# Optimization experiments

Measured on AMD Instinct MI355X. Metric: run time of the kernel, lower is better.

The kernel has to match this reference:

```python
import jax, jax.numpy as jnp
import numpy as np

N_NODES = 50000
N_EDGES = 800000
NODE_DIM = 128
EDGE_DIM = 128
HIDDEN = 128
GATE_DIM = 2


def _mlp(x, w1, b1, w2, b2):
    # Linear -> ReLU -> Linear (assumed 2-layer MLP(in, out, hidden))
    return jax.nn.relu(x @ w1.T + b1) @ w2.T + b2


def _init_linear(key, out_d, in_d, scale=0.02):
    return (jax.random.normal(key, (out_d, in_d), dtype=jnp.float32) * scale)


def setup_inputs() -> dict:
    key = jax.random.key(0)
    ks = jax.random.split(key, 32)
    inp = {}
    inp["h_node"] = jax.random.normal(ks[0], (N_NODES, NODE_DIM), dtype=jnp.float32)
    inp["h_edge"] = jax.random.normal(ks[1], (N_EDGES, EDGE_DIM), dtype=jnp.float32)
    inp["edge_index"] = jax.random.randint(ks[2], (2, N_EDGES), 0, N_NODES, dtype=jnp.int64)
    inp["relative_vec"] = jax.random.normal(ks[3], (N_EDGES, 3), dtype=jnp.float32)
    inp["distance"] = jax.random.uniform(ks[4], (N_EDGES,), dtype=jnp.float32)
    inp["node_extra"] = jax.random.normal(ks[5], (N_NODES, GATE_DIM), dtype=jnp.float32)
    # left_lin_edge: MLP(node_dim, node_dim, hidden)
    inp["left_w1"] = _init_linear(ks[6], HIDDEN, NODE_DIM)
    inp["left_b1"] = jnp.zeros((HIDDEN,), jnp.float32)
    inp["left_w2"] = _init_linear(ks[7], NODE_DIM, HIDDEN)
    inp["left_b2"] = jnp.zeros((NODE_DIM,), jnp.float32)
    # right_lin_edge: MLP(node_dim, node_dim, hidden)
    inp["right_w1"] = _init_linear(ks[8], HIDDEN, NODE_DIM)
    inp["right_b1"] = jnp.zeros((HIDDEN,), jnp.float32)
    inp["right_w2"] = _init_linear(ks[9], NODE_DIM, HIDDEN)
    inp["right_b2"] = jnp.zeros((NODE_DIM,), jnp.float32)
    # BondFFN(edge_dim, node_dim*2, inter_dim=node_dim, gate_dim, out_dim=1)
    inp["bond_lin_w"] = _init_linear(ks[10], NODE_DIM, EDGE_DIM)           # bond_linear (no bias)
    inp["nodeb_lin_w"] = _init_linear(ks[11], NODE_DIM, 2 * NODE_DIM)      # node_linear (no bias)
    inp["inter_w1"] = _init_linear(ks[12], NODE_DIM, NODE_DIM)             # inter MLP(node_dim,1,node_dim)
    inp["inter_b1"] = jnp.zeros((NODE_DIM,), jnp.float32)
    inp["inter_w2"] = _init_linear(ks[13], 1, NODE_DIM)
    inp["inter_b2"] = jnp.zeros((1,), jnp.float32)
    gate_in = EDGE_DIM + 2 * NODE_DIM + GATE_DIM                            # 386
    inp["gate_w1"] = _init_linear(ks[14], 32, gate_in)                     # gate MLP(gate_in,1,32)
    inp["gate_b1"] = jnp.zeros((32,), jnp.float32)
    inp["gate_w2"] = _init_linear(ks[15], 1, 32)
    inp["gate_b2"] = jnp.zeros((1,), jnp.float32)
    # pos_scale_net: MLP(node_dim+1+2, 1, hidden) -> sigmoid
    inp["scale_w1"] = _init_linear(ks[16], HIDDEN, NODE_DIM + 1 + GATE_DIM)
    inp["scale_b1"] = jnp.zeros((HIDDEN,), jnp.float32)
    inp["scale_w2"] = _init_linear(ks[17], 1, HIDDEN)
    inp["scale_b2"] = jnp.zeros((1,), jnp.float32)
    return inp


def reference(h_node, h_edge, edge_index, relative_vec, distance, node_extra,
              left_w1, left_b1, left_w2, left_b2,
              right_w1, right_b1, right_w2, right_b2,
              bond_lin_w, nodeb_lin_w,
              inter_w1, inter_b1, inter_w2, inter_b2,
              gate_w1, gate_b1, gate_w2, gate_b2,
              scale_w1, scale_b1, scale_w2, scale_b2):
    el, er = edge_index[0], edge_index[1]
    # gather + per-edge node MLPs
    left_feat = _mlp(h_node[el], left_w1, left_b1, left_w2, left_b2)    # [E, node_dim]
    right_feat = _mlp(h_node[er], right_w1, right_b1, right_w2, right_b2)
    both_extra = node_extra[el]                                         # [E, gate_dim]
    node_cat = jnp.concatenate([left_feat, right_feat], axis=-1)        # [E, 2*node_dim]
    # BondFFN
    inter_feat = h_edge @ bond_lin_w.T + node_cat @ nodeb_lin_w.T       # [E, node_dim]
    inter_feat = _mlp(inter_feat, inter_w1, inter_b1, inter_w2, inter_b2)  # [E, 1]
    gate = _mlp(jnp.concatenate([h_edge, node_cat, both_extra], axis=-1),
                gate_w1, gate_b1, gate_w2, gate_b2)                     # [E, 1]
    weight_edge = inter_feat * jax.nn.sigmoid(gate)                     # [E, 1]
    d = distance[:, None]
    force_edge = weight_edge * relative_vec / (d + 1e-6) / (d + 5.0) * 5  # [E, 3]
    # scatter_sum over left node index
    delta_pos = jax.ops.segment_sum(force_edge, el, num_segments=h_node.shape[0])  # [N, 3]
    nrm = jnp.linalg.norm(delta_pos, axis=-1, keepdims=True)
    scale = jax.nn.sigmoid(_mlp(jnp.concatenate([h_node, node_extra, nrm], axis=-1),
                                scale_w1, scale_b1, scale_w2, scale_b2))  # [N, 1]
    return delta_pos * scale
```

## Files before the change

### kernel.cpp

```cpp
#include <hip/hip_runtime.h>
#include <math.h>

#define N_NODES 50000
#define N_EDGES 800000

using bf16x8 = __attribute__((ext_vector_type(8))) short;
using f32x4  = __attribute__((ext_vector_type(4))) float;
typedef unsigned short u16;
typedef unsigned int   u32;

__device__ __forceinline__ u16 f2bf(float f) {
    union { float f; u32 u; } v; v.f = f;
    u32 u = v.u + 0x7fffu + ((v.u >> 16) & 1u);
    return (u16)(u >> 16);
}
__device__ __forceinline__ float bf2f(u32 h) {
    union { u32 u; float f; } v; v.u = h << 16;
    return v.f;
}

#define SA_LD 136
#define SW_LD 40

template<bool RELU>
__global__ __launch_bounds__(256, 4)
void mfma_gemm(const u16* __restrict__ A, int lda,
               const u16* __restrict__ W, int ldw,
               const float* __restrict__ bias,
               u16* __restrict__ C, int ldc,
               int M, int N, int K)
{
    __shared__ u16 sA[64 * SW_LD];
    __shared__ u16 sW[64 * SW_LD];
    const int tid = threadIdx.x;
    const int w = tid >> 6, lane = tid & 63, lx = lane & 15, quad = lane >> 4;
    const int m0 = blockIdx.x * 64, n0 = blockIdx.y * 64;

    f32x4 acc[4];
#pragma unroll
    for (int nt = 0; nt < 4; ++nt) {
        float b = bias ? bias[n0 + nt * 16 + lx] : 0.f;
        f32x4 t; t[0] = b; t[1] = b; t[2] = b; t[3] = b; acc[nt] = t;
    }

    const int sr = tid >> 2;
    const int sseg = (tid & 3) * 8;
    const int ksteps = K >> 5;
    for (int ks = 0; ks < ksteps; ++ks) {
        const int k0 = ks * 32;
        __syncthreads();
        int am = m0 + sr; if (am >= M) am = M - 1;
        uint4 va = *(const uint4*)&A[(size_t)am * lda + k0 + sseg];
        *(uint4*)&sA[sr * SW_LD + sseg] = va;
        uint4 vw = *(const uint4*)&W[(size_t)(n0 + sr) * ldw + k0 + sseg];
        *(uint4*)&sW[sr * SW_LD + sseg] = vw;
        __syncthreads();
        bf16x8 af = *(const bf16x8*)&sA[(w * 16 + lx) * SW_LD + quad * 8];
#pragma unroll
        for (int nt = 0; nt < 4; ++nt) {
            bf16x8 bf = *(const bf16x8*)&sW[(nt * 16 + lx) * SW_LD + quad * 8];
            acc[nt] = __builtin_amdgcn_mfma_f32_16x16x32_bf16(af, bf, acc[nt], 0, 0, 0);
        }
    }
#pragma unroll
    for (int r = 0; r < 4; ++r) {
        int m = m0 + w * 16 + quad * 4 + r;
        if (m >= M) continue;
#pragma unroll
        for (int nt = 0; nt < 4; ++nt) {
            float v = acc[nt][r];
            if (RELU) v = fmaxf(v, 0.f);
            C[(size_t)m * ldc + n0 + nt * 16 + lx] = f2bf(v);
        }
    }
}

__global__ void conv_hnode(const float* __restrict__ src, u16* __restrict__ dst)
{
    int idx = blockIdx.x * 256 + threadIdx.x;
    if (idx >= N_NODES * 32) return;
    float4 v = ((const float4*)src)[idx];
    uint2 o;
    o.x = (u32)f2bf(v.x) | ((u32)f2bf(v.y) << 16);
    o.y = (u32)f2bf(v.z) | ((u32)f2bf(v.w) << 16);
    *(uint2*)&dst[(size_t)idx * 4] = o;
}

__global__ void prep_small(const float* lw1, const float* rw1,
                           const float* lb1, const float* rb1,
                           const float* bond_w, const float* iw1, const float* gw1,
                           const float* sw1,
                           u16* W1cat, float* b1cat, u16* bond_bf, u16* iw1_bf,
                           u16* gate_bf, u16* sw1c)
{
    int idx = blockIdx.x * 256 + threadIdx.x;
    if (idx < 32768) {
        int i = idx >> 7, k = idx & 127;
        float v = (i < 128) ? lw1[i * 128 + k] : rw1[(i - 128) * 128 + k];
        W1cat[idx] = f2bf(v);
    } else if (idx < 33024) {
        int i = idx - 32768;
        b1cat[i] = (i < 128) ? lb1[i] : rb1[i - 128];
    } else if (idx < 49408) {
        int t = idx - 33024;
        bond_bf[t] = f2bf(bond_w[t]);
    } else if (idx < 65792) {
        int t = idx - 49408;
        iw1_bf[t] = f2bf(iw1[t]);
    } else if (idx < 69888) {
        int t = idx - 65792;
        int g = t >> 7, k = t & 127;
        gate_bf[t] = f2bf(gw1[(size_t)g * 386 + k]);
    } else if (idx < 90368) {
        int t = idx - 69888;
        int o = t / 160, k = t % 160;
        sw1c[t] = (k < 131) ? f2bf(sw1[(size_t)o * 131 + k]) : (u16)0;
    }
}

__global__ void compose_wp(const float* __restrict__ nodeb_w, const float* __restrict__ gw1,
                           const float* __restrict__ lw2, const float* __restrict__ rw2,
                           const float* __restrict__ lb2, const float* __restrict__ rb2,
                           const float* __restrict__ gb1,
                           u16* __restrict__ WP, float* __restrict__ bP)
{
    int idx = blockIdx.x * 256 + threadIdx.x;
    if (idx >= 320 * 256) return;
    int i = idx >> 8;
    int j = idx & 255;
    bool leftRow = (i < 160);
    bool leftK = (j < 128);
    if (leftRow != leftK) { WP[idx] = 0; return; }

    const float* src;
    const float* w2 = leftRow ? lw2 : rw2;
    const float* b2 = leftRow ? lb2 : rb2;
    float biasExtra = 0.f;
    if (i < 128) {
        int c = ((i & 7) << 4) + (i >> 3);
        src = nodeb_w + (size_t)c * 256;
    } else if (i < 160) {
        int r = i - 128, g = ((r & 1) << 4) + (r >> 1);
        src = gw1 + (size_t)g * 386 + 128;
        biasExtra = gb1[g];
    } else if (i < 288) {
        int r = i - 160, c = ((r & 7) << 4) + (r >> 3);
        src = nodeb_w + (size_t)c * 256 + 128;
    } else {
        int r = i - 288, g = ((r & 1) << 4) + (r >> 1);
        src = gw1 + (size_t)g * 386 + 256;
    }
    int jj = j & 127;
    float s = 0.f;
#pragma unroll 4
    for (int k = 0; k < 128; ++k)
        s += src[k] * w2[(size_t)k * 128 + jj];
    WP[idx] = f2bf(s);
    if (jj == 0) {
        float b = biasExtra;
        for (int k = 0; k < 128; ++k) b += src[k] * b2[k];
        bP[i] = b;
    }
}

__global__ void fix_glx(u16* __restrict__ P, const float* __restrict__ ne,
                        const float* __restrict__ gw1)
{
    int idx = blockIdx.x * 256 + threadIdx.x;
    if (idx >= N_NODES * 32) return;
    int n = idx >> 5, g = idx & 31;
    int pos = ((g & 15) << 1) + (g >> 4);
    u16* p = &P[(size_t)n * 320 + 128 + pos];
    float v = bf2f(*p) + ne[n * 2] * gw1[(size_t)g * 386 + 384]
                       + ne[n * 2 + 1] * gw1[(size_t)g * 386 + 385];
    *p = f2bf(v);
}

__global__ __launch_bounds__(256, 4)
void edge_kernel(const float* __restrict__ he,
                 const int*   __restrict__ eidx,
                 const float* __restrict__ rel_vec,
                 const float* __restrict__ dist,
                 const u16*   __restrict__ P,
                 const u16*   __restrict__ bondw,
                 const u16*   __restrict__ iw1w,
                 const u16*   __restrict__ gatew,
                 const float* __restrict__ ib1,
                 const float* __restrict__ iw2,
                 const float* __restrict__ ib2,
                 const float* __restrict__ gw2,
                 const float* __restrict__ gb2,
                 float* __restrict__ dp)
{
    __shared__ u16 sA[64 * SA_LD];
    __shared__ u16 sW[128 * SW_LD];
    __shared__ u16 sWg[32 * SW_LD];
    __shared__ int sEL[64], sER[64];
    __shared__ float sG[64], sIS[64];

    const int tid = threadIdx.x;
    const int w = tid >> 6, lane = tid & 63, lx = lane & 15, quad = lane >> 4;
    const int eb = blockIdx.x * 64;

    if (tid < 64) { sEL[tid] = eidx[eb + tid]; sER[tid] = eidx[N_EDGES + eb + tid]; }

#pragma unroll
    for (int j = 0; j < 8; ++j) {
        int fid = j * 256 + tid;
        int e = fid >> 5, kq = (fid & 31) << 2;
        float4 v = *(const float4*)&he[(size_t)(eb + e) * 128 + kq];
        uint2 o;
        o.x = (u32)f2bf(v.x) | ((u32)f2bf(v.y) << 16);
        o.y = (u32)f2bf(v.z) | ((u32)f2bf(v.w) << 16);
        *(uint2*)&sA[e * SA_LD + kq] = o;
    }

    f32x4 acc[8], accg[2];
#pragma unroll
    for (int i = 0; i < 8; ++i) { f32x4 z; z[0]=0;z[1]=0;z[2]=0;z[3]=0; acc[i] = z; }
    { f32x4 z; z[0]=0;z[1]=0;z[2]=0;z[3]=0; accg[0] = z; accg[1] = z; }

    const int wrow = tid >> 1;
    const int wseg = (tid & 1) * 16;

    for (int ks = 0; ks < 4; ++ks) {
        const int k0 = ks * 32;
        __syncthreads();
        {
            uint4 v0 = *(const uint4*)&bondw[wrow * 128 + k0 + wseg];
            uint4 v1 = *(const uint4*)&bondw[wrow * 128 + k0 + wseg + 8];
            *(uint4*)&sW[wrow * SW_LD + wseg] = v0;
            *(uint4*)&sW[wrow * SW_LD + wseg + 8] = v1;
            if (tid < 64) {
                uint4 g0 = *(const uint4*)&gatew[wrow * 128 + k0 + wseg];
                uint4 g1 = *(const uint4*)&gatew[wrow * 128 + k0 + wseg + 8];
                *(uint4*)&sWg[wrow * SW_LD + wseg] = g0;
                *(uint4*)&sWg[wrow * SW_LD + wseg + 8] = g1;
            }
        }
        __syncthreads();
        bf16x8 af = *(const bf16x8*)&sA[(w * 16 + lx) * SA_LD + k0 + quad * 8];
#pragma unroll
        for (int nt = 0; nt < 8; ++nt) {
            bf16x8 bf = *(const bf16x8*)&sW[(nt * 16 + lx) * SW_LD + quad * 8];
            acc[nt] = __builtin_amdgcn_mfma_f32_16x16x32_bf16(af, bf, acc[nt], 0, 0, 0);
        }
#pragma unroll
        for (int nt = 0; nt < 2; ++nt) {
            bf16x8 bf = *(const bf16x8*)&sWg[(nt * 16 + lx) * SW_LD + quad * 8];
            accg[nt] = __builtin_amdgcn_mfma_f32_16x16x32_bf16(af, bf, accg[nt], 0, 0, 0);
        }
    }

    {
        float gw2a = gw2[lx], gw2b = gw2[16 + lx];
        float gb2v = gb2[0];
#pragma unroll
        for (int r = 0; r < 4; ++r) {
            int erow = w * 16 + quad * 4 + r;
            size_t lbase = (size_t)sEL[erow] * 320;
            size_t rbase = (size_t)sER[erow] * 320 + 160;
            u32 gl = *(const u32*)&P[lbase + 128 + lx * 2];
            u32 gr = *(const u32*)&P[rbase + 128 + lx * 2];
            float g0 = bf2f(gl & 0xffff) + bf2f(gr & 0xffff);
            float g1 = bf2f(gl >> 16) + bf2f(gr >> 16);
            float v = fmaxf(accg[0][r] + g0, 0.f) * gw2a
                    + fmaxf(accg[1][r] + g1, 0.f) * gw2b;
            v += __shfl_xor(v, 1); v += __shfl_xor(v, 2);
            v += __shfl_xor(v, 4); v += __shfl_xor(v, 8);
            if (lx == 0) sG[erow] = 1.f / (1.f + __expf(-(v + gb2v)));
        }
    }

    __syncthreads();

#pragma unroll
    for (int r = 0; r < 4; ++r) {
        int erow = w * 16 + quad * 4 + r;
        size_t lbase = (size_t)sEL[erow] * 320;
        size_t rbase = (size_t)sER[erow] * 320 + 160;
        uint4 lv = *(const uint4*)&P[lbase + lx * 8];
        uint4 rv = *(const uint4*)&P[rbase + lx * 8];
        const u32* lw_ = (const u32*)&lv;
        const u32* rw_ = (const u32*)&rv;
#pragma unroll
        for (int nt = 0; nt < 8; ++nt) {
            u32 lh = (nt & 1) ? (lw_[nt >> 1] >> 16) : (lw_[nt >> 1] & 0xffff);
            u32 rh = (nt & 1) ? (rw_[nt >> 1] >> 16) : (rw_[nt >> 1] & 0xffff);
            float tv = acc[nt][r] + bf2f(lh) + bf2f(rh);
            sA[erow * SA_LD + nt * 16 + lx] = f2bf(tv);
        }
    }
#pragma unroll
    for (int nt = 0; nt < 8; ++nt) {
        float b = ib1[nt * 16 + lx];
        f32x4 t; t[0] = b; t[1] = b; t[2] = b; t[3] = b; acc[nt] = t;
    }
    __syncthreads();

    for (int ks = 0; ks < 4; ++ks) {
        const int k0 = ks * 32;
        __syncthreads();
        {
            uint4 v0 = *(const uint4*)&iw1w[wrow * 128 + k0 + wseg];
            uint4 v1 = *(const uint4*)&iw1w[wrow * 128 + k0 + wseg + 8];
            *(uint4*)&sW[wrow * SW_LD + wseg] = v0;
            *(uint4*)&sW[wrow * SW_LD + wseg + 8] = v1;
        }
        __syncthreads();
        bf16x8 af = *(const bf16x8*)&sA[(w * 16 + lx) * SA_LD + k0 + quad * 8];
#pragma unroll
        for (int nt = 0; nt < 8; ++nt) {
            bf16x8 bf = *(const bf16x8*)&sW[(nt * 16 + lx) * SW_LD + quad * 8];
            acc[nt] = __builtin_amdgcn_mfma_f32_16x16x32_bf16(af, bf, acc[nt], 0, 0, 0);
        }
    }

    {
        float ib2v = ib2[0];
        float iw2v[8];
#pragma unroll
        for (int nt = 0; nt < 8; ++nt) iw2v[nt] = iw2[nt * 16 + lx];
#pragma unroll
        for (int r = 0; r < 4; ++r) {
            float v = 0.f;
#pragma unroll
            for (int nt = 0; nt < 8; ++nt)
                v += fmaxf(acc[nt][r], 0.f) * iw2v[nt];
            v += __shfl_xor(v, 1); v += __shfl_xor(v, 2);
            v += __shfl_xor(v, 4); v += __shfl_xor(v, 8);
            if (lx == 0) sIS[w * 16 + quad * 4 + r] = v + ib2v;
        }
    }
    __syncthreads();

    if (tid < 64) {
        float wgt = sIS[tid] * sG[tid];
        float d = dist[eb + tid];
        float coef = 5.f * wgt / ((d + 1e-6f) * (d + 5.f));
        const float* rv = &rel_vec[(size_t)(eb + tid) * 3];
        int n = sEL[tid];
        atomicAdd(&dp[n * 3 + 0], coef * rv[0]);
        atomicAdd(&dp[n * 3 + 1], coef * rv[1]);
        atomicAdd(&dp[n * 3 + 2], coef * rv[2]);
    }
}

__global__ void build_xc(u16* __restrict__ Xc, const float* __restrict__ h_node,
                         const float* __restrict__ ne, const float* __restrict__ dp)
{
    int idx = blockIdx.x * 256 + threadIdx.x;
    if (idx >= N_NODES * 160) return;
    int n = idx / 160, c = idx % 160;
    float v;
    if (c < 128) v = h_node[(size_t)n * 128 + c];
    else if (c == 128) v = ne[n * 2];
    else if (c == 129) v = ne[n * 2 + 1];
    else if (c == 130) {
        float x = dp[n * 3], y = dp[n * 3 + 1], z = dp[n * 3 + 2];
        v = sqrtf(x * x + y * y + z * z);
    } else v = 0.f;
    Xc[idx] = f2bf(v);
}

__global__ __launch_bounds__(256)
void finalize(const u16* __restrict__ U, const float* __restrict__ sw2,
              const float* __restrict__ sb2, const float* __restrict__ dp,
              float* __restrict__ out)
{
    int node = blockIdx.x * 4 + (threadIdx.x >> 6);
    int lane = threadIdx.x & 63;
    const u16* u = &U[(size_t)node * 128];
    float p = bf2f(u[lane]) * sw2[lane] + bf2f(u[lane + 64]) * sw2[lane + 64];
    p += __shfl_xor(p, 1);  p += __shfl_xor(p, 2);
    p += __shfl_xor(p, 4);  p += __shfl_xor(p, 8);
    p += __shfl_xor(p, 16); p += __shfl_xor(p, 32);
    if (lane == 0) {
        float s = 1.f / (1.f + __expf(-(p + sb2[0])));
        out[node * 3 + 0] = dp[node * 3 + 0] * s;
        out[node * 3 + 1] = dp[node * 3 + 1] * s;
        out[node * 3 + 2] = dp[node * 3 + 2] * s;
    }
}

extern "C" void kernel_launch(void* const* d_in, const int* in_sizes, int n_in,
                              void* d_out, int out_size, void* d_ws, size_t ws_size,
                              hipStream_t stream)
{
    const float* h_node  = (const float*)d_in[0];
    const float* h_edge  = (const float*)d_in[1];
    const int*   eidx    = (const int*)  d_in[2];
    const float* rel_vec = (const float*)d_in[3];
    const float* dist    = (const float*)d_in[4];
    const float* ne      = (const float*)d_in[5];
    const float* lw1 = (const float*)d_in[6];  const float* lb1 = (const float*)d_in[7];
    const float* lw2 = (const float*)d_in[8];  const float* lb2 = (const float*)d_in[9];
    const float* rw1 = (const float*)d_in[10]; const float* rb1 = (const float*)d_in[11];
    const float* rw2 = (const float*)d_in[12]; const float* rb2 = (const float*)d_in[13];
    const float* bond_w  = (const float*)d_in[14];
    const float* nodeb_w = (const float*)d_in[15];
    const float* iw1 = (const float*)d_in[16]; const float* ib1 = (const float*)d_in[17];
    const float* iw2 = (const float*)d_in[18]; const float* ib2 = (const float*)d_in[19];
    const float* gw1 = (const float*)d_in[20]; const float* gb1 = (const float*)d_in[21];
    const float* gw2 = (const float*)d_in[22]; const float* gb2 = (const float*)d_in[23];
    const float* sw1 = (const float*)d_in[24]; const float* sb1 = (const float*)d_in[25];
    const float* sw2 = (const float*)d_in[26]; const float* sb2 = (const float*)d_in[27];
    float* out = (float*)d_out;

    char* base = (char*)d_ws;
    auto carve = [&](size_t bytes) { char* p = base; base += (bytes + 255) & ~(size_t)255; return p; };
    u16*  hnode_bf = (u16*) carve((size_t)N_NODES * 128 * 2);
    u16*  H1       = (u16*) carve((size_t)N_NODES * 256 * 2);
    u16*  P        = (u16*) carve((size_t)N_NODES * 320 * 2);
    u16*  Xc       = (u16*) carve((size_t)N_NODES * 160 * 2);
    u16*  U        = (u16*) carve((size_t)N_NODES * 128 * 2);
    u16*  W1cat    = (u16*) carve(256 * 128 * 2);
    u16*  WP       = (u16*) carve(320 * 256 * 2);
    u16*  bond_bf  = (u16*) carve(128 * 128 * 2);
    u16*  iw1_bf   = (u16*) carve(128 * 128 * 2);
    u16*  gate_bf  = (u16*) carve(32 * 128 * 2);
    u16*  sw1c     = (u16*) carve(128 * 160 * 2);
    float* b1cat   = (float*)carve(256 * 4);
    float* bP      = (float*)carve(320 * 4);
    float* dp      = (float*)carve((size_t)N_NODES * 3 * 4);

    hipMemsetAsync(dp, 0, (size_t)N_NODES * 3 * 4, stream);

    dim3 blk(256);
    conv_hnode<<<(N_NODES * 32 + 255) / 256, blk, 0, stream>>>(h_node, hnode_bf);
    prep_small<<<(90368 + 255) / 256, blk, 0, stream>>>(lw1, rw1, lb1, rb1, bond_w, iw1, gw1, sw1,
                                                        W1cat, b1cat, bond_bf, iw1_bf, gate_bf, sw1c);
    compose_wp<<<320, blk, 0, stream>>>(nodeb_w, gw1, lw2, rw2, lb2, rb2, gb1, WP, bP);

    const int MB = (N_NODES + 63) / 64;
    mfma_gemm<true ><<<dim3(MB, 4), blk, 0, stream>>>(hnode_bf, 128, W1cat, 128, b1cat, H1, 256, N_NODES, 256, 128);
    mfma_gemm<false><<<dim3(MB, 5), blk, 0, stream>>>(H1, 256, WP, 256, bP, P, 320, N_NODES, 320, 256);
    fix_glx<<<(N_NODES * 32 + 255) / 256, blk, 0, stream>>>(P, ne, gw1);

    edge_kernel<<<N_EDGES / 64, blk, 0, stream>>>(h_edge, eidx, rel_vec, dist, P,
                                                  bond_bf, iw1_bf, gate_bf,
                                                  ib1, iw2, ib2, gw2, gb2, dp);

    build_xc<<<(N_NODES * 160 + 255) / 256, blk, 0, stream>>>(Xc, h_node, ne, dp);
    mfma_gemm<true ><<<dim3(MB, 2), blk, 0, stream>>>(Xc, 160, sw1c, 160, sb1, U, 128, N_NODES, 128, 160);
    finalize<<<N_NODES / 4, blk, 0, stream>>>(U, sw2, sb2, dp, out);
}
```

Measured before the change: 839.5 us.

## Pre-swizzle edge weights to MFMA fragment layout and load whole matrices once

The bond, inter and gate weight matrices are stored in a fragment-ordered layout so each lane reads contiguous 16-byte chunks. Each matrix is loaded into shared memory once per block, which removes the per-k-step syncs and reloads. The edge block grows to 128 edges with 512 threads, and the gathers of node features from P are issued early so they overlap the first GEMM. The scatter is split across three threads per edge, one per coordinate. This raises LDS usage per block and register pressure, which may lower occupancy.

```diff
diff --git a/kernel.cpp b/kernel.cpp
--- a/kernel.cpp
+++ b/kernel.cpp
@@ -103,14 +103,22 @@
         b1cat[i] = (i < 128) ? lb1[i] : rb1[i - 128];
     } else if (idx < 49408) {
         int t = idx - 33024;
-        bond_bf[t] = f2bf(bond_w[t]);
+        int e = t & 7, lx = (t >> 3) & 15, quad = (t >> 7) & 3;
+        int ks = (t >> 9) & 3, g = t >> 11;
+        int n = g * 16 + lx, k = ks * 32 + quad * 8 + e;
+        bond_bf[t] = f2bf(bond_w[n * 128 + k]);
     } else if (idx < 65792) {
         int t = idx - 49408;
-        iw1_bf[t] = f2bf(iw1[t]);
+        int e = t & 7, lx = (t >> 3) & 15, quad = (t >> 7) & 3;
+        int ks = (t >> 9) & 3, g = t >> 11;
+        int n = g * 16 + lx, k = ks * 32 + quad * 8 + e;
+        iw1_bf[t] = f2bf(iw1[n * 128 + k]);
     } else if (idx < 69888) {
         int t = idx - 65792;
-        int g = t >> 7, k = t & 127;
-        gate_bf[t] = f2bf(gw1[(size_t)g * 386 + k]);
+        int e = t & 7, lx = (t >> 3) & 15, quad = (t >> 7) & 3;
+        int ks = (t >> 9) & 3, g = t >> 11;
+        int n = g * 16 + lx, k = ks * 32 + quad * 8 + e;
+        gate_bf[t] = f2bf(gw1[(size_t)n * 386 + k]);
     } else if (idx < 90368) {
         int t = idx - 69888;
         int o = t / 160, k = t % 160;
@@ -176,7 +184,7 @@
     *p = f2bf(v);
 }
 
-__global__ __launch_bounds__(256, 4)
+__global__ __launch_bounds__(512, 4)
 void edge_kernel(const float* __restrict__ he,
                  const int*   __restrict__ eidx,
                  const float* __restrict__ rel_vec,
@@ -192,21 +200,27 @@
                  const float* __restrict__ gb2,
                  float* __restrict__ dp)
 {
-    __shared__ u16 sA[64 * SA_LD];
-    __shared__ u16 sW[128 * SW_LD];
-    __shared__ u16 sWg[32 * SW_LD];
-    __shared__ int sEL[64], sER[64];
-    __shared__ float sG[64], sIS[64];
+    __shared__ u16 sA[128 * SA_LD];
+    __shared__ u16 sW[16384 + 4096];
+    __shared__ int sEL[128], sER[128];
+    __shared__ float sG[128], sIS[128];
 
     const int tid = threadIdx.x;
     const int w = tid >> 6, lane = tid & 63, lx = lane & 15, quad = lane >> 4;
-    const int eb = blockIdx.x * 64;
-
-    if (tid < 64) { sEL[tid] = eidx[eb + tid]; sER[tid] = eidx[N_EDGES + eb + tid]; }
+    const int eb = blockIdx.x * 128;
+
+    if (tid < 128) { sEL[tid] = eidx[eb + tid]; sER[tid] = eidx[N_EDGES + eb + tid]; }
+
+#pragma unroll
+    for (int j = 0; j < 4; ++j) {
+        int t = j * 512 + tid;
+        *(uint4*)&sW[t * 8] = *(const uint4*)&bondw[t * 8];
+    }
+    *(uint4*)&sW[16384 + tid * 8] = *(const uint4*)&gatew[tid * 8];
 
 #pragma unroll
     for (int j = 0; j < 8; ++j) {
-        int fid = j * 256 + tid;
+        int fid = j * 512 + tid;
         int e = fid >> 5, kq = (fid & 31) << 2;
         float4 v = *(const float4*)&he[(size_t)(eb + e) * 128 + kq];
         uint2 o;
@@ -214,40 +228,36 @@
         o.y = (u32)f2bf(v.z) | ((u32)f2bf(v.w) << 16);
         *(uint2*)&sA[e * SA_LD + kq] = o;
     }
+    __syncthreads();
+
+    uint4 lv[4], rv[4]; u32 gl[4], gr[4];
+#pragma unroll
+    for (int r = 0; r < 4; ++r) {
+        int erow = w * 16 + quad * 4 + r;
+        size_t lbase = (size_t)sEL[erow] * 320;
+        size_t rbase = (size_t)sER[erow] * 320 + 160;
+        lv[r] = *(const uint4*)&P[lbase + lx * 8];
+        rv[r] = *(const uint4*)&P[rbase + lx * 8];
+        gl[r] = *(const u32*)&P[lbase + 128 + lx * 2];
+        gr[r] = *(const u32*)&P[rbase + 128 + lx * 2];
+    }
 
     f32x4 acc[8], accg[2];
 #pragma unroll
     for (int i = 0; i < 8; ++i) { f32x4 z; z[0]=0;z[1]=0;z[2]=0;z[3]=0; acc[i] = z; }
     { f32x4 z; z[0]=0;z[1]=0;z[2]=0;z[3]=0; accg[0] = z; accg[1] = z; }
 
-    const int wrow = tid >> 1;
-    const int wseg = (tid & 1) * 16;
-
+#pragma unroll
     for (int ks = 0; ks < 4; ++ks) {
-        const int k0 = ks * 32;
-        __syncthreads();
-        {
-            uint4 v0 = *(const uint4*)&bondw[wrow * 128 + k0 + wseg];
-            uint4 v1 = *(const uint4*)&bondw[wrow * 128 + k0 + wseg + 8];
-            *(uint4*)&sW[wrow * SW_LD + wseg] = v0;
-            *(uint4*)&sW[wrow * SW_LD + wseg + 8] = v1;
-            if (tid < 64) {
-                uint4 g0 = *(const uint4*)&gatew[wrow * 128 + k0 + wseg];
-                uint4 g1 = *(const uint4*)&gatew[wrow * 128 + k0 + wseg + 8];
-                *(uint4*)&sWg[wrow * SW_LD + wseg] = g0;
-                *(uint4*)&sWg[wrow * SW_LD + wseg + 8] = g1;
-            }
-        }
-        __syncthreads();
-        bf16x8 af = *(const bf16x8*)&sA[(w * 16 + lx) * SA_LD + k0 + quad * 8];
+        bf16x8 af = *(const bf16x8*)&sA[(w * 16 + lx) * SA_LD + ks * 32 + quad * 8];
 #pragma unroll
         for (int nt = 0; nt < 8; ++nt) {
-            bf16x8 bf = *(const bf16x8*)&sW[(nt * 16 + lx) * SW_LD + quad * 8];
+            bf16x8 bf = *(const bf16x8*)&sW[((nt * 4 + ks) << 9) + lane * 8];
             acc[nt] = __builtin_amdgcn_mfma_f32_16x16x32_bf16(af, bf, acc[nt], 0, 0, 0);
         }
 #pragma unroll
         for (int nt = 0; nt < 2; ++nt) {
-            bf16x8 bf = *(const bf16x8*)&sWg[(nt * 16 + lx) * SW_LD + quad * 8];
+            bf16x8 bf = *(const bf16x8*)&sW[16384 + ((nt * 4 + ks) << 9) + lane * 8];
             accg[nt] = __builtin_amdgcn_mfma_f32_16x16x32_bf16(af, bf, accg[nt], 0, 0, 0);
         }
     }
@@ -257,32 +267,21 @@
         float gb2v = gb2[0];
 #pragma unroll
         for (int r = 0; r < 4; ++r) {
-            int erow = w * 16 + quad * 4 + r;
-            size_t lbase = (size_t)sEL[erow] * 320;
-            size_t rbase = (size_t)sER[erow] * 320 + 160;
-            u32 gl = *(const u32*)&P[lbase + 128 + lx * 2];
-            u32 gr = *(const u32*)&P[rbase + 128 + lx * 2];
-            float g0 = bf2f(gl & 0xffff) + bf2f(gr & 0xffff);
-            float g1 = bf2f(gl >> 16) + bf2f(gr >> 16);
+            float g0 = bf2f(gl[r] & 0xffff) + bf2f(gr[r] & 0xffff);
+            float g1 = bf2f(gl[r] >> 16) + bf2f(gr[r] >> 16);
             float v = fmaxf(accg[0][r] + g0, 0.f) * gw2a
                     + fmaxf(accg[1][r] + g1, 0.f) * gw2b;
             v += __shfl_xor(v, 1); v += __shfl_xor(v, 2);
             v += __shfl_xor(v, 4); v += __shfl_xor(v, 8);
-            if (lx == 0) sG[erow] = 1.f / (1.f + __expf(-(v + gb2v)));
-        }
-    }
-
-    __syncthreads();
+            if (lx == 0) sG[w * 16 + quad * 4 + r] = 1.f / (1.f + __expf(-(v + gb2v)));
+        }
+    }
 
 #pragma unroll
     for (int r = 0; r < 4; ++r) {
         int erow = w * 16 + quad * 4 + r;
-        size_t lbase = (size_t)sEL[erow] * 320;
-        size_t rbase = (size_t)sER[erow] * 320 + 160;
-        uint4 lv = *(const uint4*)&P[lbase + lx * 8];
-        uint4 rv = *(const uint4*)&P[rbase + lx * 8];
-        const u32* lw_ = (const u32*)&lv;
-        const u32* rw_ = (const u32*)&rv;
+        const u32* lw_ = (const u32*)&lv[r];
+        const u32* rw_ = (const u32*)&rv[r];
 #pragma unroll
         for (int nt = 0; nt < 8; ++nt) {
             u32 lh = (nt & 1) ? (lw_[nt >> 1] >> 16) : (lw_[nt >> 1] & 0xffff);
@@ -296,22 +295,21 @@
         float b = ib1[nt * 16 + lx];
         f32x4 t; t[0] = b; t[1] = b; t[2] = b; t[3] = b; acc[nt] = t;
     }
+
     __syncthreads();
-
+#pragma unroll
+    for (int j = 0; j < 4; ++j) {
+        int t = j * 512 + tid;
+        *(uint4*)&sW[t * 8] = *(const uint4*)&iw1w[t * 8];
+    }
+    __syncthreads();
+
+#pragma unroll
     for (int ks = 0; ks < 4; ++ks) {
-        const int k0 = ks * 32;
-        __syncthreads();
-        {
-            uint4 v0 = *(const uint4*)&iw1w[wrow * 128 + k0 + wseg];
-            uint4 v1 = *(const uint4*)&iw1w[wrow * 128 + k0 + wseg + 8];
-            *(uint4*)&sW[wrow * SW_LD + wseg] = v0;
-            *(uint4*)&sW[wrow * SW_LD + wseg + 8] = v1;
-        }
-        __syncthreads();
-        bf16x8 af = *(const bf16x8*)&sA[(w * 16 + lx) * SA_LD + k0 + quad * 8];
+        bf16x8 af = *(const bf16x8*)&sA[(w * 16 + lx) * SA_LD + ks * 32 + quad * 8];
 #pragma unroll
         for (int nt = 0; nt < 8; ++nt) {
-            bf16x8 bf = *(const bf16x8*)&sW[(nt * 16 + lx) * SW_LD + quad * 8];
+            bf16x8 bf = *(const bf16x8*)&sW[((nt * 4 + ks) << 9) + lane * 8];
             acc[nt] = __builtin_amdgcn_mfma_f32_16x16x32_bf16(af, bf, acc[nt], 0, 0, 0);
         }
     }
@@ -334,15 +332,14 @@
     }
     __syncthreads();
 
-    if (tid < 64) {
-        float wgt = sIS[tid] * sG[tid];
-        float d = dist[eb + tid];
-        float coef = 5.f * wgt / ((d + 1e-6f) * (d + 5.f));
-        const float* rv = &rel_vec[(size_t)(eb + tid) * 3];
-        int n = sEL[tid];
-        atomicAdd(&dp[n * 3 + 0], coef * rv[0]);
-        atomicAdd(&dp[n * 3 + 1], coef * rv[1]);
-        atomicAdd(&dp[n * 3 + 2], coef * rv[2]);
+    {
+        int e = tid >> 2, c = tid & 3;
+        if (c < 3) {
+            float wgt = sIS[e] * sG[e];
+            float d = dist[eb + e];
+            float coef = 5.f * wgt / ((d + 1e-6f) * (d + 5.f));
+            atomicAdd(&dp[sEL[e] * 3 + c], coef * rel_vec[(size_t)(eb + e) * 3 + c]);
+        }
     }
 }
 
@@ -437,9 +434,9 @@
     mfma_gemm<false><<<dim3(MB, 5), blk, 0, stream>>>(H1, 256, WP, 256, bP, P, 320, N_NODES, 320, 256);
     fix_glx<<<(N_NODES * 32 + 255) / 256, blk, 0, stream>>>(P, ne, gw1);
 
-    edge_kernel<<<N_EDGES / 64, blk, 0, stream>>>(h_edge, eidx, rel_vec, dist, P,
-                                                  bond_bf, iw1_bf, gate_bf,
-                                                  ib1, iw2, ib2, gw2, gb2, dp);
+    edge_kernel<<<N_EDGES / 128, dim3(512), 0, stream>>>(h_edge, eidx, rel_vec, dist, P,
+                                                         bond_bf, iw1_bf, gate_bf,
+                                                         ib1, iw2, ib2, gw2, gb2, dp);
 
     build_xc<<<(N_NODES * 160 + 255) / 256, blk, 0, stream>>>(Xc, h_node, ne, dp);
     mfma_gemm<true ><<<dim3(MB, 2), blk, 0, stream>>>(Xc, 160, sw1c, 160, sb1, U, 128, N_NODES, 128, 160);
```

Result: faster. 818.1 us (-2.5%).
